# Optimization experiments

Hardware: AMD Instinct MI355X
Metric: run time of the kernel (lower is better)

Reference implementation:

```python
import jax, jax.numpy as jnp
import numpy as np

N_NODES = 100000
N_EDGES = 1600000
HID = 128
N_GRAPHS = 2048


def _glorot(key, shape):
    fan_in, fan_out = shape[0], shape[1]
    lim = (6.0 / (fan_in + fan_out)) ** 0.5
    return jax.random.uniform(key, shape, jnp.float32, -lim, lim)


def setup_inputs() -> dict:
    key = jax.random.key(0)
    ks = jax.random.split(key, 16)
    x = jax.random.normal(ks[0], (N_NODES, 1), jnp.float32)
    edge_index = jax.random.randint(ks[1], (2, N_EDGES), 0, N_NODES, jnp.int64)
    batch = jnp.sort(jax.random.randint(ks[2], (N_NODES,), 0, N_GRAPHS, jnp.int64))
    return {
        "x": x,
        "edge_index": edge_index,
        "batch": batch,
        "W1": _glorot(ks[3], (1, HID)),   "b1": jnp.zeros((HID,), jnp.float32),
        "W2": _glorot(ks[4], (HID, HID)), "b2": jnp.zeros((HID,), jnp.float32),
        "W3": _glorot(ks[5], (HID, HID)), "b3": jnp.zeros((HID,), jnp.float32),
        "Wl1": _glorot(ks[6], (HID, HID)), "bl1": jnp.zeros((HID,), jnp.float32),
        "Wl2": _glorot(ks[7], (HID, HID)), "bl2": jnp.zeros((HID,), jnp.float32),
        "Wl3": _glorot(ks[8], (HID, 1)),   "bl3": jnp.zeros((1,), jnp.float32),
    }


def _gcn_layer(h, src, dst, norm, W, b, n_nodes):
    # h: [N, Fin] -> [N, Fout]; GCNConv: D^-1/2 (A+I) D^-1/2 (h W) + b
    hw = h @ W                                   # [N, Fout]
    msg = hw[src] * norm[:, None]                # [E+N, Fout] gather + scale
    return jax.ops.segment_sum(msg, dst, num_segments=n_nodes) + b


def _gcn_norm(edge_index, n_nodes, dtype):
    loop = jnp.arange(n_nodes, dtype=edge_index.dtype)
    src = jnp.concatenate([edge_index[0], loop])  # self-loops appended
    dst = jnp.concatenate([edge_index[1], loop])
    deg = jax.ops.segment_sum(jnp.ones_like(dst, dtype=dtype), dst, num_segments=n_nodes)
    dinv = jnp.where(deg > 0, jax.lax.rsqrt(jnp.maximum(deg, 1e-12)), 0.0)
    norm = dinv[src] * dinv[dst]                  # [E+N]
    return src, dst, norm


def reference(x, edge_index, batch, W1, b1, W2, b2, W3, b3, Wl1, bl1, Wl2, bl2, Wl3, bl3):
    n = x.shape[0]
    src, dst, norm = _gcn_norm(edge_index, n, x.dtype)
    h = jax.nn.relu(_gcn_layer(x, src, dst, norm, W1, b1, n))
    h = jax.nn.relu(_gcn_layer(h, src, dst, norm, W2, b2, n))
    h = jax.nn.relu(_gcn_layer(h, src, dst, norm, W3, b3, n))
    # global_mean_pool over graph ids
    sums = jax.ops.segment_sum(h, batch, num_segments=N_GRAPHS)          # [G, HID]
    cnt = jax.ops.segment_sum(jnp.ones((n,), h.dtype), batch, num_segments=N_GRAPHS)
    g = sums / jnp.maximum(cnt, 1.0)[:, None]
    g = jax.nn.relu(g @ Wl1 + bl1)
    g = jax.nn.relu(g @ Wl2 + bl2)
    out = g @ Wl3 + bl3                                                  # [G, 1]
    return out.reshape(-1)
```

## Files before the change

### kernel.cpp

```cpp
#include <hip/hip_runtime.h>
#include <hip/hip_fp16.h>

#define H 128
#define SHIFT 9
#define BN 512
#define MAXNB 256
#define CHUNK 4096
#define CAP 16384

typedef _Float16 half8 __attribute__((ext_vector_type(8)));
typedef _Float16 half4 __attribute__((ext_vector_type(4)));
typedef _Float16 half2t __attribute__((ext_vector_type(2)));
typedef float f32x4 __attribute__((ext_vector_type(4)));


__global__ __launch_bounds__(256) void scatter_pairs_k(const int* __restrict__ src,
                                                       const int* __restrict__ dst,
                                                       int* __restrict__ gcur,
                                                       unsigned* __restrict__ pairbuf,
                                                       int E, int NBv) {
    __shared__ unsigned stage[CHUNK];
    __shared__ unsigned char stb[CHUNK];
    __shared__ int hist[MAXNB], basel[MAXNB], cur[MAXNB], gbase[MAXNB];
    __shared__ int total;
    int tid = threadIdx.x;
    int base = blockIdx.x * CHUNK;

    int mysrc[16], mydst[16];
    #pragma unroll
    for (int i = 0; i < 16; ++i) {
        int e = base + i * 256 + tid;
        if (e < E) { mysrc[i] = src[e]; mydst[i] = dst[e]; } else mydst[i] = -1;
    }
    hist[tid] = 0;
    __syncthreads();
    #pragma unroll
    for (int i = 0; i < 16; ++i)
        if (mydst[i] >= 0) atomicAdd(&hist[mydst[i] >> SHIFT], 1);
    __syncthreads();
    if (tid == 0) {
        int run = 0;
        for (int b = 0; b < NBv; ++b) { basel[b] = run; run += hist[b]; }
        total = run;
    }
    __syncthreads();
    if (tid < NBv) {
        cur[tid] = basel[tid];
        if (hist[tid] > 0) gbase[tid] = tid * CAP + atomicAdd(&gcur[tid], hist[tid]);
    }
    __syncthreads();
    #pragma unroll
    for (int i = 0; i < 16; ++i)
        if (mydst[i] >= 0) {
            int b = mydst[i] >> SHIFT;
            int slot = atomicAdd(&cur[b], 1);
            stage[slot] = ((unsigned)(mydst[i] & (BN - 1)) << 17) | (unsigned)mysrc[i];
            stb[slot] = (unsigned char)b;
        }
    __syncthreads();
    for (int s = tid; s < total; s += 256) {
        int b = stb[s];
        pairbuf[gbase[b] + (s - basel[b])] = stage[s];
    }
}

__global__ __launch_bounds__(512) void build_csr_k(const unsigned* __restrict__ pairbuf,
                                                   const int* __restrict__ gcur,
                                                   const float* __restrict__ x,
                                                   int* __restrict__ offs, int* __restrict__ eend,
                                                   float* __restrict__ dinv, float* __restrict__ s,
                                                   int* __restrict__ csr, int N) {
    __shared__ int hist[BN];
    __shared__ int cur[BN];
    __shared__ int ps[BN];
    int b = blockIdx.x, tid = threadIdx.x;
    int node0 = b << SHIFT;
    int e0 = b * CAP, e1 = e0 + gcur[b];
    hist[tid] = 0;
    __syncthreads();
    for (int p = e0 + tid; p < e1; p += 512)
        atomicAdd(&hist[pairbuf[p] >> 17], 1);
    __syncthreads();
    int v0 = hist[tid];
    ps[tid] = v0;
    __syncthreads();
    for (int off = 1; off < BN; off <<= 1) {
        int t = (tid >= off) ? ps[tid - off] : 0;
        __syncthreads();
        ps[tid] += t;
        __syncthreads();
    }
    int g0 = e0 + ps[tid] - v0;
    int n0 = node0 + tid;
    if (n0 < N) {
        float d = rsqrtf((float)(v0 + 1));
        offs[n0] = g0;
        eend[n0] = g0 + v0;
        dinv[n0] = d;
        s[n0] = x[n0] * d;
    }
    cur[tid] = g0;
    __syncthreads();
    for (int p = e0 + tid; p < e1; p += 512) {
        unsigned v = pairbuf[p];
        int pos = atomicAdd(&cur[v >> 17], 1);
        csr[pos] = (int)(v & 0x1FFFFu);
    }
}


__global__ __launch_bounds__(256) void agg1_k(const float* __restrict__ s, const int* __restrict__ offs,
                                              const int* __restrict__ eend, const int* __restrict__ csr,
                                              const float* __restrict__ dinv, float2* __restrict__ td, int n) {
    int l = threadIdx.x & 63;
    int wave = threadIdx.x >> 6;
    int sub = l >> 4;
    int j   = l & 15;
    int node = blockIdx.x * 16 + wave * 4 + sub;
    int nd = node < n ? node : n - 1;
    int e0 = offs[nd], e1 = eend[nd];
    float sum = 0.f;
    int p = e0 + j;
    for (; p + 16 < e1; p += 32) {
        int iA = csr[p];
        int iB = csr[p + 16];
        float vA = s[iA];
        float vB = s[iB];
        sum += vA + vB;
    }
    if (p < e1) sum += s[csr[p]];
    #pragma unroll
    for (int m = 1; m < 16; m <<= 1) sum += __shfl_xor(sum, m);
    if (j == 0 && node < n) {
        float d = dinv[nd];
        td[node] = make_float2((sum + s[nd]) * d, d);
    }
}


__global__ __launch_bounds__(256) void gather_td_k(const int* __restrict__ csr,
                                                   const float2* __restrict__ td,
                                                   const int* __restrict__ gcur,
                                                   float2* __restrict__ etd) {
    int b = blockIdx.x >> 2;
    int k = blockIdx.x & 3;
    int base = b * CAP + k * (CAP / 4);
    int e1 = b * CAP + gcur[b];
    int hi = base + (CAP / 4); if (hi > e1) hi = e1;
    for (int p0 = base; p0 < hi; p0 += 1024) {
        int p = p0 + threadIdx.x;
        bool m0 = (p < hi), m1 = (p + 256 < hi), m2 = (p + 512 < hi), m3 = (p + 768 < hi);
        int i0 = m0 ? csr[p] : 0;
        int i1 = m1 ? csr[p + 256] : 0;
        int i2 = m2 ? csr[p + 512] : 0;
        int i3 = m3 ? csr[p + 768] : 0;
        float2 v0 = td[i0];
        float2 v1 = td[i1];
        float2 v2 = td[i2];
        float2 v3 = td[i3];
        if (m0) etd[p] = v0;
        if (m1) etd[p + 256] = v1;
        if (m2) etd[p + 512] = v2;
        if (m3) etd[p + 768] = v3;
    }
}


__global__ __launch_bounds__(256) void l2_agg_k(const float2* __restrict__ td,
                                                const float2* __restrict__ etd,
                                                const int* __restrict__ offs,
                                                const int* __restrict__ eend,
                                                const float* __restrict__ w1,
                                                const float* __restrict__ b1,
                                                _Float16* __restrict__ Uh, int n) {
    int node = blockIdx.x * 4 + (threadIdx.x >> 6);
    int lane = threadIdx.x & 63;
    if (node >= n) return;
    float wa = w1[lane],      wb = w1[lane + 64];
    float ba = b1[lane],      bb = b1[lane + 64];
    float2 self = td[node];
    float sa = fmaxf(fmaf(self.x, wa, ba), 0.f) * self.y;
    float sb = fmaxf(fmaf(self.x, wb, bb), 0.f) * self.y;
    const float2* ep = etd + offs[node];
    int cnt = eend[node] - offs[node];
    int p = 0;
    for (; p + 8 <= cnt; p += 8) {
        float2 v[8];
        #pragma unroll
        for (int u = 0; u < 8; ++u) v[u] = ep[p + u];
        #pragma unroll
        for (int u = 0; u < 8; ++u) {
            sa = fmaf(fmaxf(fmaf(v[u].x, wa, ba), 0.f), v[u].y, sa);
            sb = fmaf(fmaxf(fmaf(v[u].x, wb, bb), 0.f), v[u].y, sb);
        }
    }
    for (; p < cnt; ++p) {
        float2 v = ep[p];
        sa = fmaf(fmaxf(fmaf(v.x, wa, ba), 0.f), v.y, sa);
        sb = fmaf(fmaxf(fmaf(v.x, wb, bb), 0.f), v.y, sb);
    }
    float d = self.y;
    Uh[(size_t)node * H + lane]      = (_Float16)(sa * d);
    Uh[(size_t)node * H + lane + 64] = (_Float16)(sb * d);
}


__global__ __launch_bounds__(256) void gemm_h_k(const _Float16* __restrict__ in,
                                                const float* __restrict__ W,
                                                const float* __restrict__ bias,
                                                const float* __restrict__ pscale,
                                                _Float16* __restrict__ out, int n) {
    __shared__ _Float16 WT[128 * 136];
    __shared__ _Float16 OT[64 * 136];
    __shared__ float bsh[H];

    for (int idx = threadIdx.x; idx < 128 * 32; idx += 256) {
        int k  = idx >> 5;
        int c4 = (idx & 31) << 2;
        float4 v = *(const float4*)(W + k * H + c4);
        WT[(c4 + 0) * 136 + k] = (_Float16)v.x;
        WT[(c4 + 1) * 136 + k] = (_Float16)v.y;
        WT[(c4 + 2) * 136 + k] = (_Float16)v.z;
        WT[(c4 + 3) * 136 + k] = (_Float16)v.w;
    }
    if (threadIdx.x < H) bsh[threadIdx.x] = bias[threadIdx.x];
    __syncthreads();

    const int wave = threadIdx.x >> 6;
    const int l    = threadIdx.x & 63;
    const int lr   = l & 15;
    const int lk   = l >> 4;
    const int row0 = blockIdx.x * 64 + wave * 16;

    f32x4 acc[8];
    #pragma unroll
    for (int c = 0; c < 8; ++c) acc[c] = (f32x4){0.f, 0.f, 0.f, 0.f};

    int arow = row0 + lr; if (arow > n - 1) arow = n - 1;
    const _Float16* ap = in + (size_t)arow * H + lk * 8;

    #pragma unroll
    for (int ks = 0; ks < 4; ++ks) {
        half8 a = *(const half8*)(ap + ks * 32);
        #pragma unroll
        for (int c = 0; c < 8; ++c) {
            half8 b = *(const half8*)(WT + (c * 16 + lr) * 136 + ks * 32 + lk * 8);
            acc[c] = __builtin_amdgcn_mfma_f32_16x16x32_f16(a, b, acc[c], 0, 0, 0);
        }
    }

    #pragma unroll
    for (int r = 0; r < 4; ++r) {
        int lrow = wave * 16 + lk * 4 + r;
        int grow = blockIdx.x * 64 + lrow;
        float sc = 1.f;
        if (pscale) { int gr = grow > n - 1 ? n - 1 : grow; sc = pscale[gr]; }
        #pragma unroll
        for (int c = 0; c < 8; ++c) {
            float v = fmaxf(acc[c][r] + bsh[c * 16 + lr], 0.f) * sc;
            OT[lrow * 136 + c * 16 + lr] = (_Float16)v;
        }
    }
    __syncthreads();

    for (int idx = threadIdx.x; idx < 64 * 16; idx += 256) {
        int row = idx >> 4;
        int gr = blockIdx.x * 64 + row;
        if (gr < n)
            ((uint4*)(out + (size_t)gr * H))[idx & 15] = ((const uint4*)(OT + row * 136))[idx & 15];
    }
}


__device__ __forceinline__ void acc_h(float4& a, uint2 r) {
    __half2 h0 = *(__half2*)&r.x;
    __half2 h1 = *(__half2*)&r.y;
    float2 f0 = __half22float2(h0);
    float2 f1 = __half22float2(h1);
    a.x += f0.x; a.y += f0.y; a.z += f1.x; a.w += f1.y;
}

__device__ __forceinline__ float4 gather_row_sum_h(const uint2* __restrict__ hrow,
                                                   const int* __restrict__ csr,
                                                   int node, int e0, int e1, int half, int l) {
    float4 acc[8];
    #pragma unroll
    for (int u = 0; u < 8; ++u) acc[u] = make_float4(0.f, 0.f, 0.f, 0.f);
    if (half == 0) {
        uint2 rs = hrow[(size_t)node * 32 + l];
        acc_h(acc[0], rs);
    }
    int q = e0;
    for (; q + 15 < e1; q += 16) {
        int idx[8];
        #pragma unroll
        for (int u = 0; u < 8; ++u) idx[u] = csr[q + 2 * u + half];
        uint2 raw[8];
        #pragma unroll
        for (int u = 0; u < 8; ++u) raw[u] = hrow[(size_t)idx[u] * 32 + l];
        #pragma unroll
        for (int u = 0; u < 8; ++u) acc_h(acc[u], raw[u]);
    }
    for (; q + 7 < e1; q += 8) {
        int idx[4];
        #pragma unroll
        for (int u = 0; u < 4; ++u) idx[u] = csr[q + 2 * u + half];
        uint2 raw[4];
        #pragma unroll
        for (int u = 0; u < 4; ++u) raw[u] = hrow[(size_t)idx[u] * 32 + l];
        #pragma unroll
        for (int u = 0; u < 4; ++u) acc_h(acc[u], raw[u]);
    }
    for (; q < e1; q += 2) {
        int off = q + half;
        if (off < e1) {
            uint2 raw = hrow[(size_t)csr[off] * 32 + l];
            acc_h(acc[0], raw);
        }
    }
    float4 sum;
    sum.x = ((acc[0].x + acc[1].x) + (acc[2].x + acc[3].x)) + ((acc[4].x + acc[5].x) + (acc[6].x + acc[7].x));
    sum.y = ((acc[0].y + acc[1].y) + (acc[2].y + acc[3].y)) + ((acc[4].y + acc[5].y) + (acc[6].y + acc[7].y));
    sum.z = ((acc[0].z + acc[1].z) + (acc[2].z + acc[3].z)) + ((acc[4].z + acc[5].z) + (acc[6].z + acc[7].z));
    sum.w = ((acc[0].w + acc[1].w) + (acc[2].w + acc[3].w)) + ((acc[4].w + acc[5].w) + (acc[6].w + acc[7].w));
    sum.x += __shfl_xor(sum.x, 32);
    sum.y += __shfl_xor(sum.y, 32);
    sum.z += __shfl_xor(sum.z, 32);
    sum.w += __shfl_xor(sum.w, 32);
    return sum;
}


__global__ __launch_bounds__(256) void agg3h_k(const uint2* __restrict__ Zh, const int* __restrict__ offs,
                                               const int* __restrict__ eend, const int* __restrict__ csr,
                                               const float* __restrict__ dinv,
                                               _Float16* __restrict__ Uh, int n) {
    int node = blockIdx.x * 4 + (threadIdx.x >> 6);
    int lane = threadIdx.x & 63;
    int half = lane >> 5;
    int l = lane & 31;
    if (node >= n) return;
    float4 sum = gather_row_sum_h(Zh, csr, node, offs[node], eend[node], half, l);
    if (half == 0) {
        float d = dinv[node];
        half4 o;
        o[0] = (_Float16)(sum.x * d);
        o[1] = (_Float16)(sum.y * d);
        o[2] = (_Float16)(sum.z * d);
        o[3] = (_Float16)(sum.w * d);
        *(half4*)(Uh + (size_t)node * H + l * 4) = o;
    }
}


__global__ __launch_bounds__(64) void pool_h_k(const _Float16* __restrict__ h, const int* __restrict__ batch,
                                               float* __restrict__ P, int n, int G) {
    int g = blockIdx.x, f = threadIdx.x;
    int lo = 0, hi = n;
    while (lo < hi) { int m = (lo + hi) >> 1; if (batch[m] < g) lo = m + 1; else hi = m; }
    int s0 = lo;
    hi = n;
    while (lo < hi) { int m = (lo + hi) >> 1; if (batch[m] < g + 1) lo = m + 1; else hi = m; }
    int s1 = lo;
    const half2t* hp = (const half2t*)h;
    float a0x = 0.f, a0y = 0.f, a1x = 0.f, a1y = 0.f;
    float a2x = 0.f, a2y = 0.f, a3x = 0.f, a3y = 0.f;
    int i = s0;
    for (; i + 4 <= s1; i += 4) {
        half2t v0 = hp[(size_t)i * 64 + f];
        half2t v1 = hp[(size_t)(i + 1) * 64 + f];
        half2t v2 = hp[(size_t)(i + 2) * 64 + f];
        half2t v3 = hp[(size_t)(i + 3) * 64 + f];
        a0x += (float)v0[0]; a0y += (float)v0[1];
        a1x += (float)v1[0]; a1y += (float)v1[1];
        a2x += (float)v2[0]; a2y += (float)v2[1];
        a3x += (float)v3[0]; a3y += (float)v3[1];
    }
    for (; i < s1; ++i) {
        half2t v = hp[(size_t)i * 64 + f];
        a0x += (float)v[0]; a0y += (float)v[1];
    }
    float sx = (a0x + a1x) + (a2x + a3x);
    float sy = (a0y + a1y) + (a2y + a3y);
    float c = (float)(s1 - s0); if (c < 1.f) c = 1.f;
    P[(size_t)g * H + 2 * f]     = sx / c;
    P[(size_t)g * H + 2 * f + 1] = sy / c;
}


__global__ __launch_bounds__(256) void head_k(const float* __restrict__ P,
                                              const float* __restrict__ Wl1, const float* __restrict__ bl1,
                                              const float* __restrict__ Wl2, const float* __restrict__ bl2,
                                              const float* __restrict__ Wl3, const float* __restrict__ bl3,
                                              float* __restrict__ out, int G) {
    __shared__ float Wb[H * H];
    __shared__ float Tl[32 * 133];
    __shared__ float w3l[H];
    int tid = threadIdx.x;
    int g0 = blockIdx.x * 32;

    if (tid < 128) w3l[tid] = Wl3[tid];
    for (int i = tid; i < H * H / 4; i += 256) ((float4*)Wb)[i] = ((const float4*)Wl1)[i];
    __syncthreads();

    const int cc = tid & 7, rg = tid >> 3, c0 = cc * 16;
    int grow = g0 + rg; if (grow > G - 1) grow = G - 1;
    float acc[16];

    #pragma unroll
    for (int j = 0; j < 16; ++j) acc[j] = 0.f;
    const float4* P4 = (const float4*)P;
    for (int k4 = 0; k4 < H / 4; ++k4) {
        float4 a = P4[(size_t)grow * 32 + k4];
        const float* wbase = Wb + (k4 * 4) * H + c0;
        #pragma unroll
        for (int kk = 0; kk < 4; ++kk) {
            float w[16];
            *(float4*)(w + 0)  = *(const float4*)(wbase + kk * H + 0);
            *(float4*)(w + 4)  = *(const float4*)(wbase + kk * H + 4);
            *(float4*)(w + 8)  = *(const float4*)(wbase + kk * H + 8);
            *(float4*)(w + 12) = *(const float4*)(wbase + kk * H + 12);
            float av = ((const float*)&a)[kk];
            #pragma unroll
            for (int j = 0; j < 16; ++j)
                acc[j] = fmaf(av, w[j], acc[j]);
        }
    }
    #pragma unroll
    for (int j = 0; j < 16; ++j)
        Tl[rg * 133 + c0 + j] = fmaxf(acc[j] + bl1[c0 + j], 0.f);
    __syncthreads();
    for (int i = tid; i < H * H / 4; i += 256) ((float4*)Wb)[i] = ((const float4*)Wl2)[i];
    __syncthreads();

    #pragma unroll
    for (int j = 0; j < 16; ++j) acc[j] = 0.f;
    for (int k4 = 0; k4 < H / 4; ++k4) {
        float4 a = *(const float4*)(Tl + rg * 133 + k4 * 4);
        const float* wbase = Wb + (k4 * 4) * H + c0;
        #pragma unroll
        for (int kk = 0; kk < 4; ++kk) {
            float w[16];
            *(float4*)(w + 0)  = *(const float4*)(wbase + kk * H + 0);
            *(float4*)(w + 4)  = *(const float4*)(wbase + kk * H + 4);
            *(float4*)(w + 8)  = *(const float4*)(wbase + kk * H + 8);
            *(float4*)(w + 12) = *(const float4*)(wbase + kk * H + 12);
            float av = ((const float*)&a)[kk];
            #pragma unroll
            for (int j = 0; j < 16; ++j)
                acc[j] = fmaf(av, w[j], acc[j]);
        }
    }
    float part = 0.f;
    #pragma unroll
    for (int j = 0; j < 16; ++j)
        part += fmaxf(acc[j] + bl2[c0 + j], 0.f) * w3l[c0 + j];
    #pragma unroll
    for (int off = 1; off < 8; off <<= 1)
        part += __shfl_xor(part, off);
    if (cc == 0 && g0 + rg < G)
        out[g0 + rg] = part + bl3[0];
}


extern "C" void kernel_launch(void* const* d_in, const int* in_sizes, int n_in,
                              void* d_out, int out_size, void* d_ws, size_t ws_size,
                              hipStream_t stream) {
    const float* x     = (const float*)d_in[0];
    const int*   ei    = (const int*)d_in[1];
    const int*   batch = (const int*)d_in[2];
    const float* W1  = (const float*)d_in[3];  const float* b1  = (const float*)d_in[4];
    const float* W2  = (const float*)d_in[5];  const float* b2  = (const float*)d_in[6];
    const float* W3  = (const float*)d_in[7];  const float* b3  = (const float*)d_in[8];
    const float* Wl1 = (const float*)d_in[9];  const float* bl1 = (const float*)d_in[10];
    const float* Wl2 = (const float*)d_in[11]; const float* bl2 = (const float*)d_in[12];
    const float* Wl3 = (const float*)d_in[13]; const float* bl3 = (const float*)d_in[14];

    const int N = in_sizes[0];
    const int E = in_sizes[1] / 2;
    const int G = out_size;
    const int* srcp = ei;
    const int* dstp = ei + E;
    const int NB = (N + BN - 1) / BN;

    char* w = (char*)d_ws;
    size_t off = 0;
    auto alloc = [&](size_t bytes) -> void* {
        void* p = w + off;
        off += (bytes + 255) & ~(size_t)255;
        return p;
    };
    int*    gcur   = (int*)alloc((size_t)MAXNB * 4);
    int*    offs   = (int*)alloc((size_t)N * 4);
    int*    eend   = (int*)alloc((size_t)N * 4);
    int*    csr    = (int*)alloc((size_t)NB * CAP * 4);
    float*  dinv   = (float*)alloc((size_t)N * 4);
    float*  sbuf   = (float*)alloc((size_t)N * 4);
    float2* td     = (float2*)alloc((size_t)N * 8);
    float*  A      = (float*)alloc((size_t)N * H * 4);
    float*  B      = (float*)alloc((size_t)N * H * 4);
    float*  P      = (float*)alloc((size_t)G * H * 4);
    unsigned* pairbuf = (unsigned*)B;
    float2*   etd     = (float2*)B;
    _Float16* Z2h     = (_Float16*)B;
    _Float16* h3h     = (_Float16*)B;
    _Float16* U2h     = (_Float16*)A;
    _Float16* U3h     = (_Float16*)A;
    (void)ws_size; (void)n_in;

    hipMemsetAsync(gcur, 0, (size_t)MAXNB * 4, stream);
    scatter_pairs_k<<<(E + CHUNK - 1) / CHUNK, 256, 0, stream>>>(srcp, dstp, gcur, pairbuf, E, NB);
    build_csr_k<<<NB, 512, 0, stream>>>(pairbuf, gcur, x, offs, eend, dinv, sbuf, csr, N);

    agg1_k<<<(N + 15) / 16, 256, 0, stream>>>(sbuf, offs, eend, csr, dinv, td, N);

    gather_td_k<<<NB * 4, 256, 0, stream>>>(csr, td, gcur, etd);
    l2_agg_k<<<(N + 3) / 4, 256, 0, stream>>>(td, etd, offs, eend, W1, b1, U2h, N);
    gemm_h_k<<<(N + 63) / 64, 256, 0, stream>>>(U2h, W2, b2, dinv, Z2h, N);

    agg3h_k<<<(N + 3) / 4, 256, 0, stream>>>((const uint2*)Z2h, offs, eend, csr, dinv, U3h, N);
    gemm_h_k<<<(N + 63) / 64, 256, 0, stream>>>(U3h, W3, b3, nullptr, h3h, N);
    pool_h_k<<<G, 64, 0, stream>>>(h3h, batch, P, N, G);

    head_k<<<(G + 31) / 32, 256, 0, stream>>>(P, Wl1, bl1, Wl2, bl2, Wl3, bl3,
                                              (float*)d_out, G);
}
```

Before: 380.3 us.

## Fuse global mean pooling into final GEMM epilogue with atomic segment sums

The final GCN layer's GEMM now accumulates per-graph feature sums directly into the pooled buffer P with run-length atomics over the sorted batch ids, instead of writing h3 to global memory and running a separate pool kernel. The mean division moves into the head kernel, which binary-searches graph boundaries to get node counts. P is zeroed by extending the existing memset. This removes a full N×H fp16 write and read plus one launch, at the cost of float atomics, whose order makes summation nondeterministic.

```diff
diff --git a/kernel.cpp b/kernel.cpp
--- a/kernel.cpp
+++ b/kernel.cpp
@@ -205,14 +205,18 @@
 }
 
 
+template <bool POOL>
 __global__ __launch_bounds__(256) void gemm_h_k(const _Float16* __restrict__ in,
                                                 const float* __restrict__ W,
                                                 const float* __restrict__ bias,
                                                 const float* __restrict__ pscale,
-                                                _Float16* __restrict__ out, int n) {
+                                                _Float16* __restrict__ out,
+                                                const int* __restrict__ batch,
+                                                float* __restrict__ P, int n) {
     __shared__ _Float16 WT[128 * 136];
     __shared__ _Float16 OT[64 * 136];
     __shared__ float bsh[H];
+    __shared__ int bid[64];
 
     for (int idx = threadIdx.x; idx < 128 * 32; idx += 256) {
         int k  = idx >> 5;
@@ -224,6 +228,10 @@
         WT[(c4 + 3) * 136 + k] = (_Float16)v.w;
     }
     if (threadIdx.x < H) bsh[threadIdx.x] = bias[threadIdx.x];
+    if (POOL && threadIdx.x < 64) {
+        int gr = blockIdx.x * 64 + threadIdx.x;
+        bid[threadIdx.x] = (gr < n) ? batch[gr] : -1;
+    }
     __syncthreads();
 
     const int wave = threadIdx.x >> 6;
@@ -263,11 +271,27 @@
     }
     __syncthreads();
 
-    for (int idx = threadIdx.x; idx < 64 * 16; idx += 256) {
-        int row = idx >> 4;
-        int gr = blockIdx.x * 64 + row;
-        if (gr < n)
-            ((uint4*)(out + (size_t)gr * H))[idx & 15] = ((const uint4*)(OT + row * 136))[idx & 15];
+    if constexpr (POOL) {
+        int f  = threadIdx.x & 127;
+        int r0 = (threadIdx.x >> 7) * 32;
+        float acc2 = 0.f;
+        int cur = bid[r0];
+        for (int r = r0; r < r0 + 32; ++r) {
+            int b = bid[r];
+            if (b != cur) {
+                if (cur >= 0) atomicAdd(&P[(size_t)cur * H + f], acc2);
+                acc2 = 0.f; cur = b;
+            }
+            if (b >= 0) acc2 += (float)OT[r * 136 + f];
+        }
+        if (cur >= 0) atomicAdd(&P[(size_t)cur * H + f], acc2);
+    } else {
+        for (int idx = threadIdx.x; idx < 64 * 16; idx += 256) {
+            int row = idx >> 4;
+            int gr = blockIdx.x * 64 + row;
+            if (gr < n)
+                ((uint4*)(out + (size_t)gr * H))[idx & 15] = ((const uint4*)(OT + row * 136))[idx & 15];
+        }
     }
 }
 
@@ -353,58 +377,33 @@
 }
 
 
-__global__ __launch_bounds__(64) void pool_h_k(const _Float16* __restrict__ h, const int* __restrict__ batch,
-                                               float* __restrict__ P, int n, int G) {
-    int g = blockIdx.x, f = threadIdx.x;
-    int lo = 0, hi = n;
-    while (lo < hi) { int m = (lo + hi) >> 1; if (batch[m] < g) lo = m + 1; else hi = m; }
-    int s0 = lo;
-    hi = n;
-    while (lo < hi) { int m = (lo + hi) >> 1; if (batch[m] < g + 1) lo = m + 1; else hi = m; }
-    int s1 = lo;
-    const half2t* hp = (const half2t*)h;
-    float a0x = 0.f, a0y = 0.f, a1x = 0.f, a1y = 0.f;
-    float a2x = 0.f, a2y = 0.f, a3x = 0.f, a3y = 0.f;
-    int i = s0;
-    for (; i + 4 <= s1; i += 4) {
-        half2t v0 = hp[(size_t)i * 64 + f];
-        half2t v1 = hp[(size_t)(i + 1) * 64 + f];
-        half2t v2 = hp[(size_t)(i + 2) * 64 + f];
-        half2t v3 = hp[(size_t)(i + 3) * 64 + f];
-        a0x += (float)v0[0]; a0y += (float)v0[1];
-        a1x += (float)v1[0]; a1y += (float)v1[1];
-        a2x += (float)v2[0]; a2y += (float)v2[1];
-        a3x += (float)v3[0]; a3y += (float)v3[1];
-    }
-    for (; i < s1; ++i) {
-        half2t v = hp[(size_t)i * 64 + f];
-        a0x += (float)v[0]; a0y += (float)v[1];
-    }
-    float sx = (a0x + a1x) + (a2x + a3x);
-    float sy = (a0y + a1y) + (a2y + a3y);
-    float c = (float)(s1 - s0); if (c < 1.f) c = 1.f;
-    P[(size_t)g * H + 2 * f]     = sx / c;
-    P[(size_t)g * H + 2 * f + 1] = sy / c;
-}
-
-
 __global__ __launch_bounds__(256) void head_k(const float* __restrict__ P,
+                                              const int* __restrict__ batch,
                                               const float* __restrict__ Wl1, const float* __restrict__ bl1,
                                               const float* __restrict__ Wl2, const float* __restrict__ bl2,
                                               const float* __restrict__ Wl3, const float* __restrict__ bl3,
-                                              float* __restrict__ out, int G) {
+                                              float* __restrict__ out, int G, int n) {
     __shared__ float Wb[H * H];
     __shared__ float Tl[32 * 133];
     __shared__ float w3l[H];
+    __shared__ int lb[33];
     int tid = threadIdx.x;
     int g0 = blockIdx.x * 32;
 
     if (tid < 128) w3l[tid] = Wl3[tid];
+    if (tid >= 128 && tid < 161) {
+        int g = g0 + (tid - 128); if (g > G) g = G;
+        int lo = 0, hi = n;
+        while (lo < hi) { int m = (lo + hi) >> 1; if (batch[m] < g) lo = m + 1; else hi = m; }
+        lb[tid - 128] = lo;
+    }
     for (int i = tid; i < H * H / 4; i += 256) ((float4*)Wb)[i] = ((const float4*)Wl1)[i];
     __syncthreads();
 
     const int cc = tid & 7, rg = tid >> 3, c0 = cc * 16;
     int grow = g0 + rg; if (grow > G - 1) grow = G - 1;
+    int cntg = lb[rg + 1] - lb[rg];
+    float rinv = 1.f / (cntg < 1 ? 1.f : (float)cntg);
     float acc[16];
 
     #pragma unroll
@@ -412,6 +411,7 @@
     const float4* P4 = (const float4*)P;
     for (int k4 = 0; k4 < H / 4; ++k4) {
         float4 a = P4[(size_t)grow * 32 + k4];
+        a.x *= rinv; a.y *= rinv; a.z *= rinv; a.w *= rinv;
         const float* wbase = Wb + (k4 * 4) * H + c0;
         #pragma unroll
         for (int kk = 0; kk < 4; ++kk) {
@@ -491,6 +491,8 @@
         return p;
     };
     int*    gcur   = (int*)alloc((size_t)MAXNB * 4);
+    float*  P      = (float*)alloc((size_t)G * H * 4);
+    size_t  zbytes = off;
     int*    offs   = (int*)alloc((size_t)N * 4);
     int*    eend   = (int*)alloc((size_t)N * 4);
     int*    csr    = (int*)alloc((size_t)NB * CAP * 4);
@@ -499,16 +501,14 @@
     float2* td     = (float2*)alloc((size_t)N * 8);
     float*  A      = (float*)alloc((size_t)N * H * 4);
     float*  B      = (float*)alloc((size_t)N * H * 4);
-    float*  P      = (float*)alloc((size_t)G * H * 4);
     unsigned* pairbuf = (unsigned*)B;
     float2*   etd     = (float2*)B;
     _Float16* Z2h     = (_Float16*)B;
-    _Float16* h3h     = (_Float16*)B;
     _Float16* U2h     = (_Float16*)A;
     _Float16* U3h     = (_Float16*)A;
     (void)ws_size; (void)n_in;
 
-    hipMemsetAsync(gcur, 0, (size_t)MAXNB * 4, stream);
+    hipMemsetAsync(gcur, 0, zbytes, stream);
     scatter_pairs_k<<<(E + CHUNK - 1) / CHUNK, 256, 0, stream>>>(srcp, dstp, gcur, pairbuf, E, NB);
     build_csr_k<<<NB, 512, 0, stream>>>(pairbuf, gcur, x, offs, eend, dinv, sbuf, csr, N);
 
@@ -516,12 +516,11 @@
 
     gather_td_k<<<NB * 4, 256, 0, stream>>>(csr, td, gcur, etd);
     l2_agg_k<<<(N + 3) / 4, 256, 0, stream>>>(td, etd, offs, eend, W1, b1, U2h, N);
-    gemm_h_k<<<(N + 63) / 64, 256, 0, stream>>>(U2h, W2, b2, dinv, Z2h, N);
+    gemm_h_k<false><<<(N + 63) / 64, 256, 0, stream>>>(U2h, W2, b2, dinv, Z2h, nullptr, nullptr, N);
 
     agg3h_k<<<(N + 3) / 4, 256, 0, stream>>>((const uint2*)Z2h, offs, eend, csr, dinv, U3h, N);
-    gemm_h_k<<<(N + 63) / 64, 256, 0, stream>>>(U3h, W3, b3, nullptr, h3h, N);
-    pool_h_k<<<G, 64, 0, stream>>>(h3h, batch, P, N, G);
-
-    head_k<<<(G + 31) / 32, 256, 0, stream>>>(P, Wl1, bl1, Wl2, bl2, Wl3, bl3,
-                                              (float*)d_out, G);
-}
+    gemm_h_k<true><<<(N + 63) / 64, 256, 0, stream>>>(U3h, W3, b3, nullptr, nullptr, batch, P, N);
+
+    head_k<<<(G + 31) / 32, 256, 0, stream>>>(P, batch, Wl1, bl1, Wl2, bl2, Wl3, bl3,
+                                              (float*)d_out, G, N);
+}
```

New measurement: 377.4 us. Within noise of the previous version (-0.8%).
